# Kernel optimization log

Measured on AMD Instinct MI355X. Metric: run time of the kernel, lower is better.

The kernel has to match this reference:

```python
import jax, jax.numpy as jnp
import numpy as np

B, T = 256, 2048
DIM_OUT, DIM_IN = 16, 16
H = 32  # hidden_size; 4H = 128 gates (i, f, g, o, PyTorch order)


def setup_inputs() -> dict:
    key = jax.random.key(0)
    ks = jax.random.split(key, 12)
    s = 1.0 / np.sqrt(H)  # PyTorch LSTM init scale
    return {
        "output_sequence": jax.random.normal(ks[0], (B, T, DIM_OUT), jnp.float32),
        "input_sequence": jax.random.normal(ks[1], (B, T, DIM_IN), jnp.float32),
        "W_ih0": jax.random.uniform(ks[2], (2, 4 * H, DIM_IN + DIM_OUT), jnp.float32, -s, s),
        "W_hh0": jax.random.uniform(ks[3], (2, 4 * H, H), jnp.float32, -s, s),
        "b_ih0": jax.random.uniform(ks[4], (2, 4 * H), jnp.float32, -s, s),
        "b_hh0": jax.random.uniform(ks[5], (2, 4 * H), jnp.float32, -s, s),
        "W_ih1": jax.random.uniform(ks[6], (2, 4 * H, 2 * H), jnp.float32, -s, s),
        "W_hh1": jax.random.uniform(ks[7], (2, 4 * H, H), jnp.float32, -s, s),
        "b_ih1": jax.random.uniform(ks[8], (2, 4 * H), jnp.float32, -s, s),
        "b_hh1": jax.random.uniform(ks[9], (2, 4 * H), jnp.float32, -s, s),
    }


def _lstm_dir(xg, W_hh, reverse):
    # xg: [T, B, 4H] precomputed input-side gate pre-activations (incl. both biases)
    def step(carry, g):
        h, c = carry
        g = g + h @ W_hh.T
        i, f, gg, o = jnp.split(g, 4, axis=-1)
        c = jax.nn.sigmoid(f) * c + jax.nn.sigmoid(i) * jnp.tanh(gg)
        h = jax.nn.sigmoid(o) * jnp.tanh(c)
        return (h, c), h

    h0 = jnp.zeros((xg.shape[1], W_hh.shape[1]), xg.dtype)
    _, hs = jax.lax.scan(step, (h0, h0), xg, reverse=reverse)
    return hs  # [T, B, H], aligned to original time indices


def _bilstm_layer(x, W_ih, W_hh, b_ih, b_hh):
    # x: [T, B, F]; W_ih: [2, 4H, F]; direction 0 = forward, 1 = backward
    xg_f = jnp.einsum('tbf,gf->tbg', x, W_ih[0]) + b_ih[0] + b_hh[0]
    xg_b = jnp.einsum('tbf,gf->tbg', x, W_ih[1]) + b_ih[1] + b_hh[1]
    hf = _lstm_dir(xg_f, W_hh[0], reverse=False)
    hb = _lstm_dir(xg_b, W_hh[1], reverse=True)
    return jnp.concatenate([hf, hb], axis=-1)  # [T, B, 2H]


def reference(output_sequence, input_sequence, W_ih0, W_hh0, b_ih0, b_hh0,
              W_ih1, W_hh1, b_ih1, b_hh1):
    # forward(): flip input_sequence along time, concat with output_sequence
    io = jnp.concatenate([output_sequence, input_sequence[:, ::-1, :]], axis=-1)
    x = jnp.transpose(io, (1, 0, 2))  # [T, B, F] time-major for scan
    h1 = _bilstm_layer(x, W_ih0, W_hh0, b_ih0, b_hh0)
    h2 = _bilstm_layer(h1, W_ih1, W_hh1, b_ih1, b_hh1)
    return jnp.transpose(h2, (1, 0, 2))  # [B, T, 2H]
```

## Files before the change

### kernel.cpp

```cpp
#include <hip/hip_runtime.h>


#define T_LEN 2048
#define BATCH 256
#define HID   32
#define PF    8
#define REC_BLOCKS 512

__device__ __forceinline__ float frcp(float x) { return __builtin_amdgcn_rcpf(x); }
__device__ __forceinline__ float rdlane(float v, int k) {
    return __int_as_float(__builtin_amdgcn_readlane(__float_as_int(v), k));
}

template<int N>
__device__ __forceinline__ void load_row(float* dst, const float* __restrict__ src) {
#pragma unroll
    for (int i = 0; i < N / 4; ++i) {
        float4 v = reinterpret_cast<const float4*>(src)[i];
        dst[4*i+0] = v.x; dst[4*i+1] = v.y; dst[4*i+2] = v.z; dst[4*i+3] = v.w;
    }
}

template<int LAYER>
__device__ __forceinline__ void gemm_body64(
        int gb,
        const float* __restrict__ OS, const float* __restrict__ IS,
        const float* __restrict__ h1,
        const float* __restrict__ Wih, const float* __restrict__ bih,
        const float* __restrict__ bhh, float* __restrict__ xg,
        int t_base, int C)
{
    constexpr int F  = (LAYER == 0) ? 32 : 64;
    constexpr int TT = 16;
    __shared__ float xs[TT][F];
    const int l     = threadIdx.x;
    const int b     = gb & (BATCH - 1);
    const int t_idx = gb >> 8;
    const int lt0   = (t_idx >> 2) * TT;
    const int d     = (t_idx >> 1) & 1;
    const int g     = (t_idx & 1) * 64 + l;

    constexpr int TOT = TT * F;
#pragma unroll
    for (int rep = 0; rep < TOT / 64; ++rep) {
        int flat = rep * 64 + l;
        int tt = flat / F, f = flat % F;
        int tl = t_base + lt0 + tt;
        int te = d ? (T_LEN - 1 - tl) : tl;
        float v;
        if (LAYER == 0) {
            v = (f < 16) ? OS[((size_t)b * T_LEN + te) * 16 + f]
                         : IS[((size_t)b * T_LEN + (T_LEN - 1 - te)) * 16 + (f - 16)];
        } else {
            v = h1[((size_t)te * BATCH + b) * 64 + f];
        }
        xs[tt][f] = v;
    }

    float w[F];
    load_row<F>(w, Wih + ((size_t)d * 128 + g) * F);
    const float bias = bih[d * 128 + g] + bhh[d * 128 + g];
    __syncthreads();

#pragma unroll
    for (int tt = 0; tt < TT; ++tt) {
        float a0 = bias, a1 = 0.f, a2 = 0.f, a3 = 0.f;
#pragma unroll
        for (int j = 0; j < F / 4; ++j) {
            float4 x = reinterpret_cast<const float4*>(xs[tt])[j];
            a0 = fmaf(x.x, w[4*j+0], a0);
            a1 = fmaf(x.y, w[4*j+1], a1);
            a2 = fmaf(x.z, w[4*j+2], a2);
            a3 = fmaf(x.w, w[4*j+3], a3);
        }
        xg[(((size_t)d * C + (lt0 + tt)) * BATCH + b) * 128 + g] = (a0 + a1) + (a2 + a3);
    }
}

template<int LAYER>
__device__ __forceinline__ void rec_body(
        int rb, const float* __restrict__ xg, const float* __restrict__ Whh,
        float* __restrict__ outp, float* __restrict__ state,
        int t_base, int C)
{
    const int l   = threadIdx.x;
    const int b   = rb & (BATCH - 1);
    const int d   = rb >> 8;
    const bool lo = (l < HID);
    const int chain = d * BATCH + b;
    const int xl  = (l + 32) & 63;

    const float mB = lo ? -2.f : -1.f;
    const float kM = lo ?  2.f :  1.f;
    const float kA = lo ? -1.f :  0.f;

    float wa[HID], wb[HID];
    load_row<HID>(wa, Whh + ((size_t)d * 128 + l) * HID);
    load_row<HID>(wb, Whh + ((size_t)d * 128 + 64 + l) * HID);

    float c = 0.f, hj = 0.f;
    if (t_base > 0 && lo) {
        c  = state[(size_t)chain * 64 + l];
        hj = state[(size_t)chain * 64 + 32 + l];
    }
    float h[HID];
#pragma unroll
    for (int k = 0; k < HID; ++k) h[k] = rdlane(hj, k);

    const size_t STRIDE = (size_t)BATCH * 128;
    const float* xp = xg + (size_t)d * C * STRIDE + (size_t)b * 128;
    const float* pf = xp + (size_t)PF * STRIDE;

    float ra[PF], rb_[PF];
#pragma unroll
    for (int u = 0; u < PF; ++u) {
        ra[u]  = xp[(size_t)u * STRIDE + l];
        rb_[u] = xp[(size_t)u * STRIDE + 64 + l];
    }

    const int te0 = d ? (T_LEN - 1 - t_base) : t_base;
    float* op;
    ptrdiff_t ostep;
    if constexpr (LAYER == 0) {
        op = outp + ((size_t)te0 * BATCH + b) * 64 + d * HID + l;
        ostep = d ? -(ptrdiff_t)(BATCH * 64) : (ptrdiff_t)(BATCH * 64);
    } else {
        op = outp + ((size_t)b * T_LEN + te0) * 64 + d * HID + l;
        ostep = d ? (ptrdiff_t)-64 : (ptrdiff_t)64;
    }

#pragma unroll 1
    for (int tb = 0; tb < C; tb += PF) {
#pragma unroll
        for (int k = 0; k < HID; k += 4)
            asm volatile("" : "+v"(wa[k]), "+v"(wa[k+1]), "+v"(wa[k+2]), "+v"(wa[k+3]));
#pragma unroll
        for (int k = 0; k < HID; k += 4)
            asm volatile("" : "+v"(wb[k]), "+v"(wb[k+1]), "+v"(wb[k+2]), "+v"(wb[k+3]));

#pragma unroll
        for (int u = 0; u < PF; ++u) {
            const float xa = ra[u], xb = rb_[u];
            ra[u]  = pf[l];
            rb_[u] = pf[64 + l];
            pf += STRIDE;

            float a0 = xa, a1 = 0.f, a2 = 0.f, a3 = 0.f;
            float b0 = xb, b1 = 0.f, b2 = 0.f, b3 = 0.f;
#pragma unroll
            for (int k = 0; k < 8; ++k) {
                a0 = fmaf(h[k],      wa[k],      a0);
                a1 = fmaf(h[k + 8],  wa[k + 8],  a1);
                a2 = fmaf(h[k + 16], wa[k + 16], a2);
                a3 = fmaf(h[k + 24], wa[k + 24], a3);
                b0 = fmaf(h[k],      wb[k],      b0);
                b1 = fmaf(h[k + 8],  wb[k + 8],  b1);
                b2 = fmaf(h[k + 16], wb[k + 16], b2);
                b3 = fmaf(h[k + 24], wb[k + 24], b3);
            }
            const float accA = (a0 + a1) + (a2 + a3);
            const float accB = (b0 + b1) + (b2 + b3);

            const float sA = frcp(1.f + __expf(-accA));
            const float rB = frcp(1.f + __expf(mB * accB));
            const float sB = fmaf(kM, rB, kA);
            const float sf = __shfl(sA, xl);
            const float so = __shfl(sB, xl);
            c = fmaf(sf, c, sA * sB);
            const float tc = fmaf(2.f, frcp(1.f + __expf(-2.f * c)), -1.f);
            hj = so * tc;
            if (lo) *op = hj;
            op += ostep;
#pragma unroll
            for (int k = 0; k < HID; ++k) h[k] = rdlane(hj, k);
        }
    }

    if (lo) {
        state[(size_t)chain * 64 + l]      = c;
        state[(size_t)chain * 64 + 32 + l] = hj;
    }
}

template<int LAYER>
__global__ __launch_bounds__(64) void xg_gemm_k(
        const float* __restrict__ OS, const float* __restrict__ IS,
        const float* __restrict__ h1,
        const float* __restrict__ Wih, const float* __restrict__ bih,
        const float* __restrict__ bhh, float* __restrict__ xg,
        int t_base, int C)
{
    gemm_body64<LAYER>(blockIdx.x, OS, IS, h1, Wih, bih, bhh, xg, t_base, C);
}

template<int LAYER>
__global__ __launch_bounds__(64, 1) void lstm_rec_k(
        const float* __restrict__ xg, const float* __restrict__ Whh,
        float* __restrict__ outp, float* __restrict__ state,
        int t_base, int C)
{
    rec_body<LAYER>(blockIdx.x, xg, Whh, outp, state, t_base, C);
}

template<int LAYER>
__global__ __launch_bounds__(64, 1) void fused_rec_gemm(
        const float* __restrict__ OS, const float* __restrict__ IS,
        const float* __restrict__ h1,
        const float* __restrict__ Wih, const float* __restrict__ bih,
        const float* __restrict__ bhh,
        const float* __restrict__ xg_rec, float* __restrict__ xg_next,
        const float* __restrict__ Whh,
        float* __restrict__ outp, float* __restrict__ state,
        int t_base_rec, int t_base_gemm, int C)
{
    if (blockIdx.x < REC_BLOCKS) {
        __builtin_amdgcn_s_setprio(1);
        rec_body<LAYER>(blockIdx.x, xg_rec, Whh, outp, state, t_base_rec, C);
    } else {
        gemm_body64<LAYER>(blockIdx.x - REC_BLOCKS, OS, IS, h1,
                           Wih, bih, bhh, xg_next, t_base_gemm, C);
    }
}

template<int LAYER>
__global__ __launch_bounds__(64, 1) void lstm_rec(
        const float* __restrict__ OS, const float* __restrict__ IS,
        const float* __restrict__ Wih, const float* __restrict__ Whh,
        const float* __restrict__ bih, const float* __restrict__ bhh,
        const float* __restrict__ h1in, float* __restrict__ outp)
{
    constexpr int F = (LAYER == 0) ? 32 : 64;
    const int l   = threadIdx.x;
    const int b   = blockIdx.x;
    const int dir = blockIdx.y;
    const int gA  = l;
    const int gB  = 64 + l;

    float wih_a[F], wih_b[F], whh_a[HID], whh_b[HID];
    load_row<F>(wih_a, Wih + ((size_t)dir * 128 + gA) * F);
    load_row<F>(wih_b, Wih + ((size_t)dir * 128 + gB) * F);
    load_row<HID>(whh_a, Whh + ((size_t)dir * 128 + gA) * HID);
    load_row<HID>(whh_b, Whh + ((size_t)dir * 128 + gB) * HID);
    const float biasA = bih[dir * 128 + gA] + bhh[dir * 128 + gA];
    const float biasB = bih[dir * 128 + gB] + bhh[dir * 128 + gB];

    float h[HID];
#pragma unroll
    for (int k = 0; k < HID; ++k) h[k] = 0.f;
    float c = 0.f;
    const bool lo = (l < HID);

    float4 X0[F / 4], X1[F / 4];

    auto load_x = [&](float4* X, int tl) {
        const int te = dir ? (T_LEN - 1 - tl) : tl;
        if constexpr (LAYER == 0) {
            const float4* p0 = reinterpret_cast<const float4*>(OS + ((size_t)b * T_LEN + te) * 16);
            const float4* p1 = reinterpret_cast<const float4*>(IS + ((size_t)b * T_LEN + (T_LEN - 1 - te)) * 16);
#pragma unroll
            for (int i = 0; i < 4; ++i) X[i] = p0[i];
#pragma unroll
            for (int i = 0; i < 4; ++i) X[4 + i] = p1[i];
        } else {
            const float4* p = reinterpret_cast<const float4*>(h1in + ((size_t)te * BATCH + b) * 64);
#pragma unroll
            for (int i = 0; i < F / 4; ++i) X[i] = p[i];
        }
    };

    auto step = [&](int tl, const float4* X) {
        const int te = dir ? (T_LEN - 1 - tl) : tl;
        float accA = biasA, accB = biasB;
#pragma unroll
        for (int i = 0; i < F / 4; ++i) {
            accA = fmaf(X[i].x, wih_a[4*i+0], accA);
            accA = fmaf(X[i].y, wih_a[4*i+1], accA);
            accA = fmaf(X[i].z, wih_a[4*i+2], accA);
            accA = fmaf(X[i].w, wih_a[4*i+3], accA);
            accB = fmaf(X[i].x, wih_b[4*i+0], accB);
            accB = fmaf(X[i].y, wih_b[4*i+1], accB);
            accB = fmaf(X[i].z, wih_b[4*i+2], accB);
            accB = fmaf(X[i].w, wih_b[4*i+3], accB);
        }
#pragma unroll
        for (int k = 0; k < HID; ++k) {
            accA = fmaf(h[k], whh_a[k], accA);
            accB = fmaf(h[k], whh_b[k], accB);
        }
        float sA = frcp(1.f + __expf(-accA));
        float argB = lo ? (-2.f * accB) : (-accB);
        float rB = frcp(1.f + __expf(argB));
        float sB = lo ? fmaf(2.f, rB, -1.f) : rB;
        float sf = __shfl(sA, (l + 32) & 63);
        float so = __shfl(sB, (l + 32) & 63);
        c = fmaf(sf, c, sA * sB);
        float tc = fmaf(2.f, frcp(1.f + __expf(-2.f * c)), -1.f);
        float hj = so * tc;
        if (lo) {
            if constexpr (LAYER == 0)
                outp[((size_t)te * BATCH + b) * 64 + dir * HID + l] = hj;
            else
                outp[((size_t)b * T_LEN + te) * 64 + dir * HID + l] = hj;
        }
#pragma unroll
        for (int k = 0; k < HID; ++k) h[k] = rdlane(hj, k);
    };

    load_x(X0, 0);
#pragma unroll 1
    for (int tt = 0; tt < T_LEN; tt += 2) {
        load_x(X1, tt + 1);
        step(tt, X0);
        int nx = tt + 2; if (nx > T_LEN - 1) nx = T_LEN - 1;
        load_x(X0, nx);
        step(tt + 1, X1);
    }
}

extern "C" void kernel_launch(void* const* d_in, const int* in_sizes, int n_in,
                              void* d_out, int out_size, void* d_ws, size_t ws_size,
                              hipStream_t stream) {
    const float* OS    = (const float*)d_in[0];
    const float* IS    = (const float*)d_in[1];
    const float* W_ih0 = (const float*)d_in[2];
    const float* W_hh0 = (const float*)d_in[3];
    const float* b_ih0 = (const float*)d_in[4];
    const float* b_hh0 = (const float*)d_in[5];
    const float* W_ih1 = (const float*)d_in[6];
    const float* W_hh1 = (const float*)d_in[7];
    const float* b_ih1 = (const float*)d_in[8];
    const float* b_hh1 = (const float*)d_in[9];
    float* out = (float*)d_out;

    const size_t H1_BYTES = (size_t)T_LEN * BATCH * 64 * sizeof(float);
    const size_t ST_BYTES = (size_t)512 * 64 * sizeof(float);
    const size_t SLACK    = (size_t)PF * BATCH * 128 * sizeof(float);

    int C = 0;
    for (int c = 512; c >= 64; c >>= 1) {
        size_t xgc = (size_t)2 * c * BATCH * 128 * sizeof(float);
        if (H1_BYTES + ST_BYTES + 2 * xgc + SLACK <= ws_size) { C = c; break; }
    }

    if (C >= 64) {
        const int NC = T_LEN / C;
        const size_t xgc = (size_t)2 * C * BATCH * 128 * sizeof(float);
        float* h1  = (float*)d_ws;
        float* st  = (float*)((char*)d_ws + H1_BYTES);
        float* xgA = (float*)((char*)d_ws + H1_BYTES + ST_BYTES);
        float* xgB = (float*)((char*)d_ws + H1_BYTES + ST_BYTES + xgc);
        float* xgbuf[2] = { xgA, xgB };

        const int GEMM_BLOCKS = (C / 16) * BATCH * 4;
        dim3 tb64(64);

        hipLaunchKernelGGL((xg_gemm_k<0>), dim3(GEMM_BLOCKS), tb64, 0, stream,
                           OS, IS, (const float*)nullptr, W_ih0, b_ih0, b_hh0,
                           xgbuf[0], 0, C);
        for (int i = 0; i < NC; ++i) {
            const float* xr = xgbuf[i & 1];
            if (i + 1 < NC) {
                hipLaunchKernelGGL((fused_rec_gemm<0>),
                                   dim3(REC_BLOCKS + GEMM_BLOCKS), tb64, 0, stream,
                                   OS, IS, (const float*)nullptr,
                                   W_ih0, b_ih0, b_hh0,
                                   xr, xgbuf[(i + 1) & 1], W_hh0,
                                   h1, st, i * C, (i + 1) * C, C);
            } else {
                hipLaunchKernelGGL((lstm_rec_k<0>), dim3(REC_BLOCKS), tb64, 0, stream,
                                   xr, W_hh0, h1, st, i * C, C);
            }
        }
        hipLaunchKernelGGL((xg_gemm_k<1>), dim3(GEMM_BLOCKS), tb64, 0, stream,
                           (const float*)nullptr, (const float*)nullptr, h1,
                           W_ih1, b_ih1, b_hh1, xgbuf[0], 0, C);
        for (int i = 0; i < NC; ++i) {
            const float* xr = xgbuf[i & 1];
            if (i + 1 < NC) {
                hipLaunchKernelGGL((fused_rec_gemm<1>),
                                   dim3(REC_BLOCKS + GEMM_BLOCKS), tb64, 0, stream,
                                   (const float*)nullptr, (const float*)nullptr, h1,
                                   W_ih1, b_ih1, b_hh1,
                                   xr, xgbuf[(i + 1) & 1], W_hh1,
                                   out, st, i * C, (i + 1) * C, C);
            } else {
                hipLaunchKernelGGL((lstm_rec_k<1>), dim3(REC_BLOCKS), tb64, 0, stream,
                                   xr, W_hh1, out, st, i * C, C);
            }
        }
    } else {
        float* h1 = (float*)d_ws;
        dim3 grid(BATCH, 2), block(64);
        hipLaunchKernelGGL((lstm_rec<0>), grid, block, 0, stream,
                           OS, IS, W_ih0, W_hh0, b_ih0, b_hh0, (const float*)nullptr, h1);
        hipLaunchKernelGGL((lstm_rec<1>), grid, block, 0, stream,
                           (const float*)nullptr, (const float*)nullptr,
                           W_ih1, W_hh1, b_ih1, b_hh1, (const float*)h1, out);
    }
}
```

Baseline: 1.921 ms.

## Pack eight wavefronts per block for recurrence and LDS-free input GEMM

Recurrent and fused kernels now launch 512-thread blocks that each run eight independent LSTM chains or GEMM tiles, one per wavefront, replacing single-wave 64-thread blocks. Inside the fused kernel the input-projection GEMM no longer stages inputs in shared memory and no longer synchronises; each wave reads its inputs straight from global memory. This is meant to reduce block scheduling overhead and let recurrence and GEMM waves share CUs more densely. In exchange, each lane now loads inputs redundantly from global memory, and the 512-thread, two-blocks-per-CU launch bound may cap registers for the recurrence, which holds large per-thread weight arrays.

```diff
diff --git a/kernel.cpp b/kernel.cpp
--- a/kernel.cpp
+++ b/kernel.cpp
@@ -5,7 +5,7 @@
 #define BATCH 256
 #define HID   32
 #define PF    8
-#define REC_BLOCKS 512
+#define REC_BLKS 64
 
 __device__ __forceinline__ float frcp(float x) { return __builtin_amdgcn_rcpf(x); }
 __device__ __forceinline__ float rdlane(float v, int k) {
@@ -78,16 +78,75 @@
 }
 
 template<int LAYER>
+__device__ __forceinline__ void gemm_body_nolds(
+        int gt, int lane,
+        const float* __restrict__ OS, const float* __restrict__ IS,
+        const float* __restrict__ h1,
+        const float* __restrict__ Wih, const float* __restrict__ bih,
+        const float* __restrict__ bhh, float* __restrict__ xg,
+        int t_base, int C)
+{
+    constexpr int F  = (LAYER == 0) ? 32 : 64;
+    constexpr int TT = 16;
+    const int b     = gt & (BATCH - 1);
+    const int t_idx = gt >> 8;
+    const int lt0   = (t_idx >> 2) * TT;
+    const int d     = (t_idx >> 1) & 1;
+    const int g     = (t_idx & 1) * 64 + lane;
+
+    float w[F];
+    load_row<F>(w, Wih + ((size_t)d * 128 + g) * F);
+    const float bias = bih[d * 128 + g] + bhh[d * 128 + g];
+
+#pragma unroll
+    for (int tt = 0; tt < TT; ++tt) {
+        const int tl = t_base + lt0 + tt;
+        const int te = d ? (T_LEN - 1 - tl) : tl;
+        float a0 = bias, a1 = 0.f, a2 = 0.f, a3 = 0.f;
+        if constexpr (LAYER == 0) {
+            const float4* p0 = reinterpret_cast<const float4*>(OS + ((size_t)b * T_LEN + te) * 16);
+            const float4* p1 = reinterpret_cast<const float4*>(IS + ((size_t)b * T_LEN + (T_LEN - 1 - te)) * 16);
+#pragma unroll
+            for (int j = 0; j < 4; ++j) {
+                float4 x = p0[j];
+                a0 = fmaf(x.x, w[4*j+0], a0);
+                a1 = fmaf(x.y, w[4*j+1], a1);
+                a2 = fmaf(x.z, w[4*j+2], a2);
+                a3 = fmaf(x.w, w[4*j+3], a3);
+            }
+#pragma unroll
+            for (int j = 0; j < 4; ++j) {
+                float4 x = p1[j];
+                a0 = fmaf(x.x, w[16+4*j+0], a0);
+                a1 = fmaf(x.y, w[16+4*j+1], a1);
+                a2 = fmaf(x.z, w[16+4*j+2], a2);
+                a3 = fmaf(x.w, w[16+4*j+3], a3);
+            }
+        } else {
+            const float4* p = reinterpret_cast<const float4*>(h1 + ((size_t)te * BATCH + b) * 64);
+#pragma unroll
+            for (int j = 0; j < 16; ++j) {
+                float4 x = p[j];
+                a0 = fmaf(x.x, w[4*j+0], a0);
+                a1 = fmaf(x.y, w[4*j+1], a1);
+                a2 = fmaf(x.z, w[4*j+2], a2);
+                a3 = fmaf(x.w, w[4*j+3], a3);
+            }
+        }
+        xg[(((size_t)d * C + (lt0 + tt)) * BATCH + b) * 128 + g] = (a0 + a1) + (a2 + a3);
+    }
+}
+
+template<int LAYER>
 __device__ __forceinline__ void rec_body(
-        int rb, const float* __restrict__ xg, const float* __restrict__ Whh,
+        int chain, int l, const float* __restrict__ xg,
+        const float* __restrict__ Whh,
         float* __restrict__ outp, float* __restrict__ state,
         int t_base, int C)
 {
-    const int l   = threadIdx.x;
-    const int b   = rb & (BATCH - 1);
-    const int d   = rb >> 8;
+    const int b   = chain & (BATCH - 1);
+    const int d   = chain >> 8;
     const bool lo = (l < HID);
-    const int chain = d * BATCH + b;
     const int xl  = (l + 32) & 63;
 
     const float mB = lo ? -2.f : -1.f;
@@ -194,16 +253,17 @@
 }
 
 template<int LAYER>
-__global__ __launch_bounds__(64, 1) void lstm_rec_k(
+__global__ __launch_bounds__(512, 2) void lstm_rec_k(
         const float* __restrict__ xg, const float* __restrict__ Whh,
         float* __restrict__ outp, float* __restrict__ state,
         int t_base, int C)
 {
-    rec_body<LAYER>(blockIdx.x, xg, Whh, outp, state, t_base, C);
-}
-
-template<int LAYER>
-__global__ __launch_bounds__(64, 1) void fused_rec_gemm(
+    const int w = threadIdx.x >> 6, l = threadIdx.x & 63;
+    rec_body<LAYER>(blockIdx.x * 8 + w, l, xg, Whh, outp, state, t_base, C);
+}
+
+template<int LAYER>
+__global__ __launch_bounds__(512, 2) void fused_rec_gemm(
         const float* __restrict__ OS, const float* __restrict__ IS,
         const float* __restrict__ h1,
         const float* __restrict__ Wih, const float* __restrict__ bih,
@@ -213,12 +273,14 @@
         float* __restrict__ outp, float* __restrict__ state,
         int t_base_rec, int t_base_gemm, int C)
 {
-    if (blockIdx.x < REC_BLOCKS) {
+    const int w = threadIdx.x >> 6, l = threadIdx.x & 63;
+    if (blockIdx.x < REC_BLKS) {
         __builtin_amdgcn_s_setprio(1);
-        rec_body<LAYER>(blockIdx.x, xg_rec, Whh, outp, state, t_base_rec, C);
+        rec_body<LAYER>(blockIdx.x * 8 + w, l, xg_rec, Whh, outp, state,
+                        t_base_rec, C);
     } else {
-        gemm_body64<LAYER>(blockIdx.x - REC_BLOCKS, OS, IS, h1,
-                           Wih, bih, bhh, xg_next, t_base_gemm, C);
+        gemm_body_nolds<LAYER>((blockIdx.x - REC_BLKS) * 8 + w, l, OS, IS, h1,
+                               Wih, bih, bhh, xg_next, t_base_gemm, C);
     }
 }
 
@@ -351,40 +413,40 @@
         float* xgB = (float*)((char*)d_ws + H1_BYTES + ST_BYTES + xgc);
         float* xgbuf[2] = { xgA, xgB };
 
-        const int GEMM_BLOCKS = (C / 16) * BATCH * 4;
-        dim3 tb64(64);
-
-        hipLaunchKernelGGL((xg_gemm_k<0>), dim3(GEMM_BLOCKS), tb64, 0, stream,
+        const int GEMM_TILES = (C / 16) * BATCH * 4;
+        dim3 tb64(64), tb512(512);
+
+        hipLaunchKernelGGL((xg_gemm_k<0>), dim3(GEMM_TILES), tb64, 0, stream,
                            OS, IS, (const float*)nullptr, W_ih0, b_ih0, b_hh0,
                            xgbuf[0], 0, C);
         for (int i = 0; i < NC; ++i) {
             const float* xr = xgbuf[i & 1];
             if (i + 1 < NC) {
                 hipLaunchKernelGGL((fused_rec_gemm<0>),
-                                   dim3(REC_BLOCKS + GEMM_BLOCKS), tb64, 0, stream,
+                                   dim3(REC_BLKS + GEMM_TILES / 8), tb512, 0, stream,
                                    OS, IS, (const float*)nullptr,
                                    W_ih0, b_ih0, b_hh0,
                                    xr, xgbuf[(i + 1) & 1], W_hh0,
                                    h1, st, i * C, (i + 1) * C, C);
             } else {
-                hipLaunchKernelGGL((lstm_rec_k<0>), dim3(REC_BLOCKS), tb64, 0, stream,
+                hipLaunchKernelGGL((lstm_rec_k<0>), dim3(REC_BLKS), tb512, 0, stream,
                                    xr, W_hh0, h1, st, i * C, C);
             }
         }
-        hipLaunchKernelGGL((xg_gemm_k<1>), dim3(GEMM_BLOCKS), tb64, 0, stream,
+        hipLaunchKernelGGL((xg_gemm_k<1>), dim3(GEMM_TILES), tb64, 0, stream,
                            (const float*)nullptr, (const float*)nullptr, h1,
                            W_ih1, b_ih1, b_hh1, xgbuf[0], 0, C);
         for (int i = 0; i < NC; ++i) {
             const float* xr = xgbuf[i & 1];
             if (i + 1 < NC) {
                 hipLaunchKernelGGL((fused_rec_gemm<1>),
-                                   dim3(REC_BLOCKS + GEMM_BLOCKS), tb64, 0, stream,
+                                   dim3(REC_BLKS + GEMM_TILES / 8), tb512, 0, stream,
                                    (const float*)nullptr, (const float*)nullptr, h1,
                                    W_ih1, b_ih1, b_hh1,
                                    xr, xgbuf[(i + 1) & 1], W_hh1,
                                    out, st, i * C, (i + 1) * C, C);
             } else {
-                hipLaunchKernelGGL((lstm_rec_k<1>), dim3(REC_BLOCKS), tb64, 0, stream,
+                hipLaunchKernelGGL((lstm_rec_k<1>), dim3(REC_BLKS), tb512, 0, stream,
                                    xr, W_hh1, out, st, i * C, C);
             }
         }
```

After: 2.766 ms. 1.44x slower.
